# Kernel optimization log

Hardware: AMD Instinct MI355X
Metric: run time of the kernel (lower is better)

The kernel has to match this reference:

```python
import jax, jax.numpy as jnp
import numpy as np

N = 2800        # real node count (before hardcoded pad)
NPAD = 3000     # module pads node dim to 3000
F_IN = 8192     # node_features
H1 = 256        # dim_h1 (GCLSTM in_channels)
H2 = 128        # GCLSTM out_channels
E = 179200      # edges (avg degree 64)


def setup_inputs() -> dict:
    key = jax.random.key(0)
    ks = jax.random.split(key, 12)
    inp = {
        "x": jax.random.normal(ks[0], (N, F_IN), jnp.float32),
        "edge_index": jax.random.randint(ks[1], (2, E), 0, N, dtype=jnp.int64),
        "edge_weight": jax.random.uniform(ks[2], (E,), jnp.float32),
        "h0": jax.random.normal(ks[3], (NPAD, H2), jnp.float32),
        "c0": jax.random.normal(ks[4], (NPAD, H2), jnp.float32),
        # fc0: node_features -> dim_h1
        "fc0_w": jax.random.normal(ks[5], (F_IN, H1), jnp.float32) / np.float32(np.sqrt(F_IN)),
        "fc0_b": jnp.zeros((H1,), jnp.float32),
        # GCLSTM gate params, stacked over gates [i, f, c, o]
        "Wx": jax.random.normal(ks[6], (4, H1, H2), jnp.float32) / np.float32(np.sqrt(H1)),
        "bg": jnp.zeros((4, H2), jnp.float32),
        # ChebConv (K=2) weights per gate: theta_0, theta_1, bias
        "cw0": jax.random.normal(ks[7], (4, H2, H2), jnp.float32) / np.float32(np.sqrt(H2)),
        "cw1": jax.random.normal(ks[8], (4, H2, H2), jnp.float32) / np.float32(np.sqrt(H2)),
        "cb": jnp.zeros((4, H2), jnp.float32),
        # final fc: 128 -> 1
        "fc_w": jax.random.normal(ks[9], (H2, 1), jnp.float32) / np.float32(np.sqrt(H2)),
        "fc_b": jnp.zeros((1,), jnp.float32),
    }
    return inp


def _cheb_scaled_laplacian(edge_index, edge_weight, num_nodes):
    # ChebConv 'sym' norm with lambda_max=2: L_hat = -D^{-1/2} A D^{-1/2}
    # (diagonal of scaled Laplacian cancels to zero with fill_value=-1 self loops)
    row, col = edge_index[0], edge_index[1]
    deg = jax.ops.segment_sum(edge_weight, row, num_segments=num_nodes)
    dinv = jnp.where(deg > 0, jax.lax.rsqrt(jnp.where(deg > 0, deg, 1.0)), 0.0)
    return -dinv[row] * edge_weight * dinv[col]  # per-edge weight of L_hat


def reference(x, edge_weight, h0, c0, fc0_w, fc0_b, Wx, bg, cw0, cw1, cb,
              fc_w, fc_b, edge_index):
    n_real = x.shape[0]
    # hardcoded zero-padding of node dim to 3000
    xp = jnp.concatenate([x, jnp.zeros((NPAD - n_real, x.shape[1]), x.dtype)], axis=0)
    z = jax.nn.relu(xp @ fc0_w + fc0_b)                       # [3000, 256]

    row, col = edge_index[0], edge_index[1]
    w_hat = _cheb_scaled_laplacian(edge_index, edge_weight, NPAD)
    # Chebyshev T1 term: L_hat @ H  (shared across all four gates)
    T1 = jax.ops.segment_sum(w_hat[:, None] * h0[row], col, num_segments=NPAD)  # [3000,128]

    # all four gate pre-activations at once: X W_x + ChebConv(H) + b
    gates = (jnp.einsum('nf,gfo->gno', z, Wx)
             + jnp.einsum('nd,gdo->gno', h0, cw0)
             + jnp.einsum('nd,gdo->gno', T1, cw1)
             + (bg + cb)[:, None, :])                          # [4, 3000, 128]

    i = jax.nn.sigmoid(gates[0])
    f = jax.nn.sigmoid(gates[1])
    t = jnp.tanh(gates[2])
    o = jax.nn.sigmoid(gates[3])
    c_new = f * c0 + i * t
    h_new = o * jnp.tanh(c_new)                                # [3000, 128]

    out = (jax.nn.relu(h_new) @ fc_w + fc_b)[:, 0]             # squeeze last dim
    out = out[:n_real]                                         # drop padding rows
    return out, h_new
```

## Files before the change

kernel.cpp:

```cpp
#include <hip/hip_runtime.h>
#include <math.h>

#define N_REAL 2800
#define NPAD   3000
#define F_IN   8192
#define H1     256
#define H2     128
#define NE     179200
#define UDIM   512
#define NGATE  512
#define MPAD   3072
#define SPLITK 16
#define KCH    (F_IN / SPLITK)
#define NHB    64
#define EPB    (NE / NHB)

typedef _Float16 half8_t __attribute__((ext_vector_type(8)));
typedef _Float16 half4_t __attribute__((ext_vector_type(4)));
typedef float    floatx4 __attribute__((ext_vector_type(4)));

__device__ __forceinline__ void async_g2l_16(const _Float16* g, _Float16* l) {
    __builtin_amdgcn_global_load_lds(
        (const __attribute__((address_space(1))) unsigned int*)g,
        (__attribute__((address_space(3))) unsigned int*)l, 16, 0, 0);
}

__global__ __launch_bounds__(256)
void prep_kernel(const float* __restrict__ w, const float* __restrict__ Wx,
                 const float* __restrict__ cw0, const float* __restrict__ cw1,
                 const float* __restrict__ bg, const float* __restrict__ cb,
                 const float* __restrict__ h0, const int* __restrict__ ei,
                 const float* __restrict__ ew,
                 _Float16* __restrict__ wTp, _Float16* __restrict__ Wcp,
                 float* __restrict__ biasv, _Float16* __restrict__ U16,
                 float* __restrict__ deg, int* __restrict__ counts,
                 int* __restrict__ cnt_pT) {
    __shared__ __align__(16) char pmem[24576];
    int b = blockIdx.x;
    int t = threadIdx.x;
    if (b < NHB) {
        float* sdeg = (float*)pmem;
        int*   scnt = (int*)(pmem + 12288);
        for (int i = t; i < 3072; i += 256) { sdeg[i] = 0.f; scnt[i] = 0; }
        __syncthreads();
        int e0 = b * EPB;
        for (int i = t; i < EPB; i += 256) {
            int e = e0 + i;
            atomicAdd(&sdeg[ei[e]], ew[e]);
            atomicAdd(&scnt[ei[NE + e]], 1);
        }
        __syncthreads();
        for (int i = t; i < 3072; i += 256) {
            atomicAdd(&deg[i], sdeg[i]);
            atomicAdd(&counts[i], scnt[i]);
            cnt_pT[i * NHB + b] = scnt[i];
        }
    } else if (b < 2112) {
        float (*tile)[33] = (float(*)[33])pmem;
        int bb = b - NHB;
        int k0 = (bb & 255) * 32;
        int n0 = (bb >> 8) * 32;
        int tx = t & 31, ty = t >> 5;
#pragma unroll
        for (int r = 0; r < 4; r++)
            tile[ty + r * 8][tx] = w[(size_t)(k0 + ty + r * 8) * H1 + n0 + tx];
        __syncthreads();
        if (t < 128) {
            int u_l = t >> 5;
            int n_l = t & 31;
            half8_t h;
#pragma unroll
            for (int j = 0; j < 8; j++) h[j] = (_Float16)tile[u_l * 8 + j][n_l];
            *(half8_t*)&wTp[(((size_t)(k0 >> 3) + u_l) * H1 + n0 + n_l) * 8] = h;
        }
    } else if (b < 3136) {
        int idx = (b - 2112) * 256 + t;
        if (idx < UDIM * NGATE) {
            int col = idx >> 9;
            int f   = idx & 511;
            int g = col >> 7, o = col & 127;
            float v;
            if (f < H1)            v = Wx[((size_t)g * H1 + f) * H2 + o];
            else if (f < H1 + H2)  v = cw0[((size_t)g * H2 + (f - H1)) * H2 + o];
            else                   v = cw1[((size_t)g * H2 + (f - H1 - H2)) * H2 + o];
            Wcp[(((size_t)(f >> 3)) * NGATE + col) * 8 + (f & 7)] = (_Float16)v;
            if (f == 0) biasv[col] = bg[col] + cb[col];
        }
    } else {
        int q = (b - 3136) * 256 + t;
        int m = q >> 5;
        int o4 = (q & 31) * 4;
        half4_t h = {};
        if (m < NPAD) {
            float4 v = *(const float4*)&h0[(size_t)m * H2 + o4];
            h[0] = (_Float16)v.x; h[1] = (_Float16)v.y; h[2] = (_Float16)v.z; h[3] = (_Float16)v.w;
        }
        *(half4_t*)&U16[(size_t)m * UDIM + H1 + o4] = h;
    }
}

__global__ __launch_bounds__(256, 3)
void gemm1_fused(const float* __restrict__ x, const _Float16* __restrict__ wTp,
                 float* __restrict__ P) {
    __shared__ __align__(16) _Float16 As[8][64][8];
    __shared__ __align__(16) _Float16 Bs[8][256][8];
    const int t = threadIdx.x;
    const int wave = t >> 6, lane = t & 63;
    const int l16 = lane & 15, u4 = lane >> 4;
    const int m0 = blockIdx.x * 64;
    const int kbase = blockIdx.y * KCH;

    const int arow = t >> 2;
    const int aseg = t & 3;
    const bool avalid = (m0 + arow) < N_REAL;
    const float* agp = x + (size_t)(m0 + arow) * F_IN + kbase + aseg * 16;

    floatx4 acc[4][4] = {};

    float4 a0 = make_float4(0.f, 0.f, 0.f, 0.f), a1 = a0, a2 = a0, a3 = a0;
    if (avalid) {
        a0 = *(const float4*)(agp + 0);
        a1 = *(const float4*)(agp + 4);
        a2 = *(const float4*)(agp + 8);
        a3 = *(const float4*)(agp + 12);
    }

    for (int kk = 0; kk < KCH; kk += 64) {
        const _Float16* bbase = wTp + ((size_t)((kbase + kk) >> 3)) * (H1 * 8);
#pragma unroll
        for (int q = 0; q < 2; q++) {
            int u = wave * 2 + q;
#pragma unroll
            for (int rg = 0; rg < 4; rg++)
                async_g2l_16(bbase + ((size_t)u * H1 + rg * 64 + lane) * 8,
                             &Bs[u][rg * 64 + lane][0]);
        }
        half8_t hlo, hhi;
        hlo[0] = (_Float16)a0.x; hlo[1] = (_Float16)a0.y; hlo[2] = (_Float16)a0.z; hlo[3] = (_Float16)a0.w;
        hlo[4] = (_Float16)a1.x; hlo[5] = (_Float16)a1.y; hlo[6] = (_Float16)a1.z; hlo[7] = (_Float16)a1.w;
        hhi[0] = (_Float16)a2.x; hhi[1] = (_Float16)a2.y; hhi[2] = (_Float16)a2.z; hhi[3] = (_Float16)a2.w;
        hhi[4] = (_Float16)a3.x; hhi[5] = (_Float16)a3.y; hhi[6] = (_Float16)a3.z; hhi[7] = (_Float16)a3.w;
        *(half8_t*)&As[aseg * 2][arow][0]     = hlo;
        *(half8_t*)&As[aseg * 2 + 1][arow][0] = hhi;
        __syncthreads();
        if (kk + 64 < KCH && avalid) {
            a0 = *(const float4*)(agp + kk + 64);
            a1 = *(const float4*)(agp + kk + 68);
            a2 = *(const float4*)(agp + kk + 72);
            a3 = *(const float4*)(agp + kk + 76);
        }
#pragma unroll
        for (int ks = 0; ks < 2; ks++) {
            half8_t a[4], bfr[4];
#pragma unroll
            for (int i = 0; i < 4; i++) a[i] = *(const half8_t*)&As[ks * 4 + u4][i * 16 + l16][0];
#pragma unroll
            for (int j = 0; j < 4; j++) bfr[j] = *(const half8_t*)&Bs[ks * 4 + u4][wave * 64 + j * 16 + l16][0];
#pragma unroll
            for (int i = 0; i < 4; i++)
#pragma unroll
                for (int j = 0; j < 4; j++)
                    acc[i][j] = __builtin_amdgcn_mfma_f32_16x16x32_f16(a[i], bfr[j], acc[i][j], 0, 0, 0);
        }
        __syncthreads();
    }

    float* Pb = P + ((size_t)blockIdx.y * MPAD + m0) * H1;
#pragma unroll
    for (int i = 0; i < 4; i++)
#pragma unroll
        for (int j = 0; j < 4; j++) {
            int n = wave * 64 + j * 16 + l16;
#pragma unroll
            for (int r = 0; r < 4; r++)
                Pb[(size_t)(i * 16 + u4 * 4 + r) * H1 + n] = acc[i][j][r];
        }
}

__device__ __forceinline__ void zreduce_body(int zb, int t, const float* __restrict__ P,
                                             const float* __restrict__ fc0_b,
                                             _Float16* __restrict__ U16) {
    int q = zb * 256 + t;
    int m = q >> 6;
    int n4 = (q & 63) * 4;
    float s0 = 0.f, s1 = 0.f, s2 = 0.f, s3 = 0.f;
#pragma unroll
    for (int sk = 0; sk < SPLITK; sk++) {
        float4 p = *(const float4*)&P[((size_t)sk * MPAD + m) * H1 + n4];
        s0 += p.x; s1 += p.y; s2 += p.z; s3 += p.w;
    }
    float4 bb = *(const float4*)&fc0_b[n4];
    half4_t h;
    h[0] = (_Float16)fmaxf(s0 + bb.x, 0.f);
    h[1] = (_Float16)fmaxf(s1 + bb.y, 0.f);
    h[2] = (_Float16)fmaxf(s2 + bb.z, 0.f);
    h[3] = (_Float16)fmaxf(s3 + bb.w, 0.f);
    *(half4_t*)&U16[(size_t)m * UDIM + n4] = h;
}

__global__ __launch_bounds__(256)
void scanz_kernel(const int* __restrict__ counts, const float* __restrict__ deg,
                  int* __restrict__ offsets, float* __restrict__ dinv,
                  const int* __restrict__ cnt_pT, int* __restrict__ base_rel,
                  const float* __restrict__ P, const float* __restrict__ fc0_b,
                  _Float16* __restrict__ U16) {
    int b = blockIdx.x;
    int t = threadIdx.x;
    if (b == 0) {
        __shared__ int wt[4];
        int i0 = t * 12;
        int v[12];
        int s = 0;
#pragma unroll
        for (int j = 0; j < 12; j++) { v[j] = counts[i0 + j]; s += v[j]; }
        int incl = s;
#pragma unroll
        for (int d = 1; d < 64; d <<= 1) {
            int n = __shfl_up(incl, d);
            if ((t & 63) >= d) incl += n;
        }
        if ((t & 63) == 63) wt[t >> 6] = incl;
        __syncthreads();
        int wbase = 0;
#pragma unroll
        for (int w = 0; w < 4; w++) wbase += (w < (t >> 6)) ? wt[w] : 0;
        int run = wbase + incl - s;
#pragma unroll
        for (int j = 0; j < 12; j++) { offsets[i0 + j] = run; run += v[j]; }
        for (int i = t; i < NPAD; i += 256) {
            float d = deg[i];
            dinv[i] = (d > 0.f) ? rsqrtf(d) : 0.f;
        }
    } else if (b <= 12) {
        int j = (b - 1) * 256 + t;
        const int* src = cnt_pT + (size_t)j * NHB;
        int* dst = base_rel + (size_t)j * NHB;
        int run = 0;
#pragma unroll
        for (int bb = 0; bb < NHB; bb++) { dst[bb] = run; run += src[bb]; }
    } else {
        zreduce_body(b - 13, t, P, fc0_b, U16);
    }
}

__global__ __launch_bounds__(256)
void scatz_kernel(const int* __restrict__ ei, const int* __restrict__ offsets,
                  const int* __restrict__ base_rel, int* __restrict__ eid,
                  const float* __restrict__ P, const float* __restrict__ fc0_b,
                  _Float16* __restrict__ U16) {
    int b = blockIdx.x;
    int t = threadIdx.x;
    if (b < NHB) {
        __shared__ int sb[3072];
        for (int j = t; j < 3072; j += 256)
            sb[j] = offsets[j] + base_rel[(size_t)j * NHB + b];
        __syncthreads();
        int e0 = b * EPB;
        for (int i = t; i < EPB; i += 256) {
            int e = e0 + i;
            int c = ei[NE + e];
            int p = atomicAdd(&sb[c], 1);
            eid[p] = e;
        }
    } else {
        zreduce_body(384 + (b - NHB), t, P, fc0_b, U16);
    }
}

__global__ __launch_bounds__(128)
void gather_kernel(const int* __restrict__ ei, const float* __restrict__ ew,
                   const float* __restrict__ h0, const float* __restrict__ dinv,
                   const int* __restrict__ offsets, const int* __restrict__ eid,
                   _Float16* __restrict__ U16) {
    __shared__ int   sr[128];
    __shared__ float sw[128];
    int n = blockIdx.x;
    int t = threadIdx.x;
    int beg = offsets[n], end = offsets[n + 1];
    float dc = dinv[n];
    float acc = 0.f;
    for (int base = beg; base < end; base += 128) {
        int j = base + t;
        if (j < end) {
            int e = eid[j];
            int r = ei[e];
            sr[t] = r;
            sw[t] = -dinv[r] * ew[e];
        }
        __syncthreads();
        int cnt = min(128, end - base);
        int k = 0;
        for (; k + 8 <= cnt; k += 8) {
            int   r0 = sr[k],   r1 = sr[k+1], r2 = sr[k+2], r3 = sr[k+3];
            int   r4 = sr[k+4], r5 = sr[k+5], r6 = sr[k+6], r7 = sr[k+7];
            float w0 = sw[k],   w1 = sw[k+1], w2 = sw[k+2], w3 = sw[k+3];
            float w4 = sw[k+4], w5 = sw[k+5], w6 = sw[k+6], w7 = sw[k+7];
            float v0 = h0[(size_t)r0 * H2 + t];
            float v1 = h0[(size_t)r1 * H2 + t];
            float v2 = h0[(size_t)r2 * H2 + t];
            float v3 = h0[(size_t)r3 * H2 + t];
            float v4 = h0[(size_t)r4 * H2 + t];
            float v5 = h0[(size_t)r5 * H2 + t];
            float v6 = h0[(size_t)r6 * H2 + t];
            float v7 = h0[(size_t)r7 * H2 + t];
            acc += w0 * v0 + w1 * v1 + w2 * v2 + w3 * v3
                 + w4 * v4 + w5 * v5 + w6 * v6 + w7 * v7;
        }
        for (; k < cnt; k++)
            acc += sw[k] * h0[(size_t)sr[k] * H2 + t];
        __syncthreads();
    }
    U16[(size_t)n * UDIM + H1 + H2 + t] = (_Float16)(acc * dc);
}

__global__ __launch_bounds__(256, 3)
void gemm2_mfma(const _Float16* __restrict__ U16, const _Float16* __restrict__ Wcp,
                float* __restrict__ gatesP) {
    __shared__ __align__(16) _Float16 As[8][64][8];
    __shared__ __align__(16) _Float16 Bs[8][256][8];
    const int t = threadIdx.x;
    const int wave = t >> 6, lane = t & 63;
    const int l16 = lane & 15, u4 = lane >> 4;
    const int n0 = blockIdx.x * 256;
    const int m0 = blockIdx.y * 64;
    const int kz = blockIdx.z * 256;

    floatx4 acc[4][4] = {};

    for (int kk = kz; kk < kz + 256; kk += 64) {
        const _Float16* bbase = Wcp + ((size_t)(kk >> 3)) * (NGATE * 8);
#pragma unroll
        for (int q = 0; q < 2; q++) {
            int u = wave * 2 + q;
            async_g2l_16(U16 + (size_t)(m0 + lane) * UDIM + kk + u * 8, &As[u][lane][0]);
#pragma unroll
            for (int rg = 0; rg < 4; rg++)
                async_g2l_16(bbase + ((size_t)u * NGATE + n0 + rg * 64 + lane) * 8,
                             &Bs[u][rg * 64 + lane][0]);
        }
        __syncthreads();
#pragma unroll
        for (int ks = 0; ks < 2; ks++) {
            half8_t a[4], bfr[4];
#pragma unroll
            for (int i = 0; i < 4; i++) a[i] = *(const half8_t*)&As[ks * 4 + u4][i * 16 + l16][0];
#pragma unroll
            for (int j = 0; j < 4; j++) bfr[j] = *(const half8_t*)&Bs[ks * 4 + u4][wave * 64 + j * 16 + l16][0];
#pragma unroll
            for (int i = 0; i < 4; i++)
#pragma unroll
                for (int j = 0; j < 4; j++)
                    acc[i][j] = __builtin_amdgcn_mfma_f32_16x16x32_f16(a[i], bfr[j], acc[i][j], 0, 0, 0);
        }
        __syncthreads();
    }

    float* g = gatesP + (size_t)blockIdx.z * MPAD * NGATE;
#pragma unroll
    for (int i = 0; i < 4; i++)
#pragma unroll
        for (int j = 0; j < 4; j++) {
            int n = n0 + wave * 64 + j * 16 + l16;
#pragma unroll
            for (int r = 0; r < 4; r++)
                g[(size_t)(m0 + i * 16 + u4 * 4 + r) * NGATE + n] = acc[i][j][r];
        }
}

__global__ __launch_bounds__(128)
void lstm_kernel(const float* __restrict__ gates, const float* __restrict__ c0,
                 const float* __restrict__ biasv, const float* __restrict__ fc_w,
                 const float* __restrict__ fc_b, float* __restrict__ out) {
    __shared__ float red[2];
    int n = blockIdx.x;
    int o = threadIdx.x;
    const float* g0 = gates + (size_t)n * NGATE;
    const float* g1 = g0 + (size_t)MPAD * NGATE;
    float gi = g0[o]          + g1[o]          + biasv[o];
    float gf = g0[H2 + o]     + g1[H2 + o]     + biasv[H2 + o];
    float gt = g0[2 * H2 + o] + g1[2 * H2 + o] + biasv[2 * H2 + o];
    float go = g0[3 * H2 + o] + g1[3 * H2 + o] + biasv[3 * H2 + o];
    float iv = 1.f / (1.f + expf(-gi));
    float fv = 1.f / (1.f + expf(-gf));
    float tv = tanhf(gt);
    float ov = 1.f / (1.f + expf(-go));
    float c = fv * c0[(size_t)n * H2 + o] + iv * tv;
    float h = ov * tanhf(c);
    out[N_REAL + (size_t)n * H2 + o] = h;

    float r = fmaxf(h, 0.f) * fc_w[o];
#pragma unroll
    for (int s = 32; s; s >>= 1) r += __shfl_down(r, s);
    if ((o & 63) == 0) red[o >> 6] = r;
    __syncthreads();
    if (o == 0 && n < N_REAL) out[n] = red[0] + red[1] + fc_b[0];
}

extern "C" void kernel_launch(void* const* d_in, const int* in_sizes, int n_in,
                              void* d_out, int out_size, void* d_ws, size_t ws_size,
                              hipStream_t stream) {
    const float* x     = (const float*)d_in[0];
    const int*   ei    = (const int*)d_in[1];
    const float* ew    = (const float*)d_in[2];
    const float* h0    = (const float*)d_in[3];
    const float* c0    = (const float*)d_in[4];
    const float* fc0_w = (const float*)d_in[5];
    const float* fc0_b = (const float*)d_in[6];
    const float* Wx    = (const float*)d_in[7];
    const float* bg    = (const float*)d_in[8];
    const float* cw0   = (const float*)d_in[9];
    const float* cw1   = (const float*)d_in[10];
    const float* cb    = (const float*)d_in[11];
    const float* fc_w  = (const float*)d_in[12];
    const float* fc_b  = (const float*)d_in[13];
    float* out = (float*)d_out;

    float* P        = (float*)d_ws;
    float* gates    = P + (size_t)SPLITK * MPAD * H1;
    float* biasv    = gates + 2 * (size_t)MPAD * NGATE;
    float* dinv     = biasv + NGATE;
    float* deg      = dinv + 3072;
    int*   counts   = (int*)(deg + 3072);
    int*   offs     = counts + 3072;
    int*   cnt_pT   = offs + 3072;
    int*   base_rel = cnt_pT + 3072 * NHB;
    int*   eid      = base_rel + 3072 * NHB;
    _Float16* U16 = (_Float16*)(((uintptr_t)(eid + NE) + 255) & ~(uintptr_t)255);
    _Float16* Wcp = U16 + (size_t)MPAD * UDIM;
    _Float16* wTp = Wcp + (size_t)UDIM * NGATE;

    hipMemsetAsync(deg, 0, 2 * 3072 * sizeof(float), stream);
    prep_kernel<<<3520, 256, 0, stream>>>(fc0_w, Wx, cw0, cw1, bg, cb, h0, ei, ew,
                                          wTp, Wcp, biasv, U16, deg, counts, cnt_pT);
    gemm1_fused<<<dim3(MPAD / 64, SPLITK), 256, 0, stream>>>(x, wTp, P);
    scanz_kernel<<<397, 256, 0, stream>>>(counts, deg, offs, dinv, cnt_pT, base_rel, P, fc0_b, U16);
    scatz_kernel<<<NHB + 384, 256, 0, stream>>>(ei, offs, base_rel, eid, P, fc0_b, U16);
    gather_kernel<<<NPAD, 128, 0, stream>>>(ei, ew, h0, dinv, offs, eid, U16);
    gemm2_mfma<<<dim3(NGATE / 256, MPAD / 64, 2), 256, 0, stream>>>(U16, Wcp, gates);
    lstm_kernel<<<NPAD, 128, 0, stream>>>(gates, c0, biasv, fc_w, fc_b, out);
}
```

Before: 242.9 us.

## Double-buffer gemm1, halve split-K, merge scan/scatter, fuse gemm2 with LSTM

The fc0 GEMM now uses double-buffered LDS with deeper A prefetch, and split-K drops from 16 to 8, which halves partial-sum traffic but also halves the number of blocks. The scan and scatter kernels are merged into one launch: each scatter block recomputes its own base from the per-block counts, so the base_rel buffer and one kernel launch go away. The gate GEMM now covers all 512 columns and the full K per block, and the LSTM pointwise math and final fc run in its epilogue from LDS. This removes the gates round-trip through global memory and the separate LSTM launch, at the cost of only 48 blocks at one block per CU for gemm2.

Measured after the change: 305.2 us. 1.26x slower.

```diff
diff --git a/kernel.cpp b/kernel.cpp
--- a/kernel.cpp
+++ b/kernel.cpp
@@ -10,7 +10,7 @@
 #define UDIM   512
 #define NGATE  512
 #define MPAD   3072
-#define SPLITK 16
+#define SPLITK 8
 #define KCH    (F_IN / SPLITK)
 #define NHB    64
 #define EPB    (NE / NHB)
@@ -99,11 +99,56 @@
     }
 }
 
-__global__ __launch_bounds__(256, 3)
+__device__ __forceinline__ void stage_b1(const _Float16* __restrict__ wTp,
+                                         _Float16 (*bs)[256][8], int wave, int lane, size_t kb8) {
+    const _Float16* bbase = wTp + kb8 * (H1 * 8);
+#pragma unroll
+    for (int q = 0; q < 2; q++) {
+        int u = wave * 2 + q;
+#pragma unroll
+        for (int rg = 0; rg < 4; rg++)
+            async_g2l_16(bbase + ((size_t)u * H1 + rg * 64 + lane) * 8,
+                         &bs[u][rg * 64 + lane][0]);
+    }
+}
+
+__device__ __forceinline__ void put_a1(_Float16 (*as)[64][8], int arow, int aseg,
+                                       const float4* A) {
+    half8_t hlo, hhi;
+    hlo[0] = (_Float16)A[0].x; hlo[1] = (_Float16)A[0].y; hlo[2] = (_Float16)A[0].z; hlo[3] = (_Float16)A[0].w;
+    hlo[4] = (_Float16)A[1].x; hlo[5] = (_Float16)A[1].y; hlo[6] = (_Float16)A[1].z; hlo[7] = (_Float16)A[1].w;
+    hhi[0] = (_Float16)A[2].x; hhi[1] = (_Float16)A[2].y; hhi[2] = (_Float16)A[2].z; hhi[3] = (_Float16)A[2].w;
+    hhi[4] = (_Float16)A[3].x; hhi[5] = (_Float16)A[3].y; hhi[6] = (_Float16)A[3].z; hhi[7] = (_Float16)A[3].w;
+    *(half8_t*)&as[aseg * 2][arow][0]     = hlo;
+    *(half8_t*)&as[aseg * 2 + 1][arow][0] = hhi;
+}
+
+__device__ __forceinline__ void comp64(floatx4 (&acc)[4][4], _Float16 (*as)[64][8],
+                                       _Float16 (*bs)[256][8], int wave, int u4, int l16) {
+#pragma unroll
+    for (int ks = 0; ks < 2; ks++) {
+        half8_t a[4], bfr[4];
+#pragma unroll
+        for (int i = 0; i < 4; i++) a[i] = *(const half8_t*)&as[ks * 4 + u4][i * 16 + l16][0];
+#pragma unroll
+        for (int j = 0; j < 4; j++) bfr[j] = *(const half8_t*)&bs[ks * 4 + u4][wave * 64 + j * 16 + l16][0];
+#pragma unroll
+        for (int i = 0; i < 4; i++)
+#pragma unroll
+            for (int j = 0; j < 4; j++)
+                acc[i][j] = __builtin_amdgcn_mfma_f32_16x16x32_f16(a[i], bfr[j], acc[i][j], 0, 0, 0);
+    }
+}
+
+#define LOADA1(A, off) do { if (avalid) { \
+    A[0] = *(const float4*)(agp + (off));      A[1] = *(const float4*)(agp + (off) + 4); \
+    A[2] = *(const float4*)(agp + (off) + 8);  A[3] = *(const float4*)(agp + (off) + 12); } } while (0)
+
+__global__ __launch_bounds__(256, 2)
 void gemm1_fused(const float* __restrict__ x, const _Float16* __restrict__ wTp,
                  float* __restrict__ P) {
-    __shared__ __align__(16) _Float16 As[8][64][8];
-    __shared__ __align__(16) _Float16 Bs[8][256][8];
+    __shared__ __align__(16) _Float16 As[2][8][64][8];
+    __shared__ __align__(16) _Float16 Bs[2][8][256][8];
     const int t = threadIdx.x;
     const int wave = t >> 6, lane = t & 63;
     const int l16 = lane & 15, u4 = lane >> 4;
@@ -116,52 +161,28 @@
     const float* agp = x + (size_t)(m0 + arow) * F_IN + kbase + aseg * 16;
 
     floatx4 acc[4][4] = {};
-
-    float4 a0 = make_float4(0.f, 0.f, 0.f, 0.f), a1 = a0, a2 = a0, a3 = a0;
-    if (avalid) {
-        a0 = *(const float4*)(agp + 0);
-        a1 = *(const float4*)(agp + 4);
-        a2 = *(const float4*)(agp + 8);
-        a3 = *(const float4*)(agp + 12);
-    }
-
-    for (int kk = 0; kk < KCH; kk += 64) {
-        const _Float16* bbase = wTp + ((size_t)((kbase + kk) >> 3)) * (H1 * 8);
-#pragma unroll
-        for (int q = 0; q < 2; q++) {
-            int u = wave * 2 + q;
-#pragma unroll
-            for (int rg = 0; rg < 4; rg++)
-                async_g2l_16(bbase + ((size_t)u * H1 + rg * 64 + lane) * 8,
-                             &Bs[u][rg * 64 + lane][0]);
-        }
-        half8_t hlo, hhi;
-        hlo[0] = (_Float16)a0.x; hlo[1] = (_Float16)a0.y; hlo[2] = (_Float16)a0.z; hlo[3] = (_Float16)a0.w;
-        hlo[4] = (_Float16)a1.x; hlo[5] = (_Float16)a1.y; hlo[6] = (_Float16)a1.z; hlo[7] = (_Float16)a1.w;
-        hhi[0] = (_Float16)a2.x; hhi[1] = (_Float16)a2.y; hhi[2] = (_Float16)a2.z; hhi[3] = (_Float16)a2.w;
-        hhi[4] = (_Float16)a3.x; hhi[5] = (_Float16)a3.y; hhi[6] = (_Float16)a3.z; hhi[7] = (_Float16)a3.w;
-        *(half8_t*)&As[aseg * 2][arow][0]     = hlo;
-        *(half8_t*)&As[aseg * 2 + 1][arow][0] = hhi;
-        __syncthreads();
-        if (kk + 64 < KCH && avalid) {
-            a0 = *(const float4*)(agp + kk + 64);
-            a1 = *(const float4*)(agp + kk + 68);
-            a2 = *(const float4*)(agp + kk + 72);
-            a3 = *(const float4*)(agp + kk + 76);
-        }
-#pragma unroll
-        for (int ks = 0; ks < 2; ks++) {
-            half8_t a[4], bfr[4];
-#pragma unroll
-            for (int i = 0; i < 4; i++) a[i] = *(const half8_t*)&As[ks * 4 + u4][i * 16 + l16][0];
-#pragma unroll
-            for (int j = 0; j < 4; j++) bfr[j] = *(const half8_t*)&Bs[ks * 4 + u4][wave * 64 + j * 16 + l16][0];
-#pragma unroll
-            for (int i = 0; i < 4; i++)
-#pragma unroll
-                for (int j = 0; j < 4; j++)
-                    acc[i][j] = __builtin_amdgcn_mfma_f32_16x16x32_f16(a[i], bfr[j], acc[i][j], 0, 0, 0);
-        }
+    float4 A0[4] = {}, A1[4] = {};
+
+    LOADA1(A0, 0);
+    stage_b1(wTp, Bs[0], wave, lane, (size_t)kbase >> 3);
+    put_a1(As[0], arow, aseg, A0);
+    LOADA1(A1, 64);
+    LOADA1(A0, 128);
+    __syncthreads();
+
+    for (int q8 = 0; q8 < 8; ++q8) {
+        const int k = 2 * q8;
+        stage_b1(wTp, Bs[1], wave, lane, (size_t)(kbase + (k + 1) * 64) >> 3);
+        put_a1(As[1], arow, aseg, A1);
+        if (q8 < 7) LOADA1(A1, (k + 3) * 64);
+        comp64(acc, As[0], Bs[0], wave, u4, l16);
+        __syncthreads();
+        if (q8 < 7) {
+            stage_b1(wTp, Bs[0], wave, lane, (size_t)(kbase + (k + 2) * 64) >> 3);
+            put_a1(As[0], arow, aseg, A0);
+            if (q8 < 6) LOADA1(A0, (k + 4) * 64);
+        }
+        comp64(acc, As[1], Bs[1], wave, u4, l16);
         __syncthreads();
     }
 
@@ -199,18 +220,19 @@
 }
 
 __global__ __launch_bounds__(256)
-void scanz_kernel(const int* __restrict__ counts, const float* __restrict__ deg,
-                  int* __restrict__ offsets, float* __restrict__ dinv,
-                  const int* __restrict__ cnt_pT, int* __restrict__ base_rel,
-                  const float* __restrict__ P, const float* __restrict__ fc0_b,
-                  _Float16* __restrict__ U16) {
+void scatterz_kernel(const int* __restrict__ ei, const int* __restrict__ counts,
+                     const float* __restrict__ deg, const int* __restrict__ cnt_pT,
+                     int* __restrict__ offsets, float* __restrict__ dinv,
+                     int* __restrict__ eid,
+                     const float* __restrict__ P, const float* __restrict__ fc0_b,
+                     _Float16* __restrict__ U16) {
+    __shared__ int sb[3072];
+    __shared__ int wt[4];
     int b = blockIdx.x;
     int t = threadIdx.x;
-    if (b == 0) {
-        __shared__ int wt[4];
+    if (b < NHB + 1) {
         int i0 = t * 12;
-        int v[12];
-        int s = 0;
+        int v[12]; int s = 0;
 #pragma unroll
         for (int j = 0; j < 12; j++) { v[j] = counts[i0 + j]; s += v[j]; }
         int incl = s;
@@ -225,45 +247,33 @@
 #pragma unroll
         for (int w = 0; w < 4; w++) wbase += (w < (t >> 6)) ? wt[w] : 0;
         int run = wbase + incl - s;
-#pragma unroll
-        for (int j = 0; j < 12; j++) { offsets[i0 + j] = run; run += v[j]; }
-        for (int i = t; i < NPAD; i += 256) {
-            float d = deg[i];
-            dinv[i] = (d > 0.f) ? rsqrtf(d) : 0.f;
-        }
-    } else if (b <= 12) {
-        int j = (b - 1) * 256 + t;
-        const int* src = cnt_pT + (size_t)j * NHB;
-        int* dst = base_rel + (size_t)j * NHB;
-        int run = 0;
-#pragma unroll
-        for (int bb = 0; bb < NHB; bb++) { dst[bb] = run; run += src[bb]; }
+        if (b < NHB) {
+#pragma unroll
+            for (int j = 0; j < 12; j++) {
+                int base = 0;
+                const int* cp = cnt_pT + (size_t)(i0 + j) * NHB;
+                for (int bb = 0; bb < b; bb++) base += cp[bb];
+                sb[i0 + j] = run + base;
+                run += v[j];
+            }
+            __syncthreads();
+            int e0 = b * EPB;
+            for (int i = t; i < EPB; i += 256) {
+                int e = e0 + i;
+                int c = ei[NE + e];
+                int p = atomicAdd(&sb[c], 1);
+                eid[p] = e;
+            }
+        } else {
+#pragma unroll
+            for (int j = 0; j < 12; j++) { offsets[i0 + j] = run; run += v[j]; }
+            for (int i = t; i < NPAD; i += 256) {
+                float d = deg[i];
+                dinv[i] = (d > 0.f) ? rsqrtf(d) : 0.f;
+            }
+        }
     } else {
-        zreduce_body(b - 13, t, P, fc0_b, U16);
-    }
-}
-
-__global__ __launch_bounds__(256)
-void scatz_kernel(const int* __restrict__ ei, const int* __restrict__ offsets,
-                  const int* __restrict__ base_rel, int* __restrict__ eid,
-                  const float* __restrict__ P, const float* __restrict__ fc0_b,
-                  _Float16* __restrict__ U16) {
-    int b = blockIdx.x;
-    int t = threadIdx.x;
-    if (b < NHB) {
-        __shared__ int sb[3072];
-        for (int j = t; j < 3072; j += 256)
-            sb[j] = offsets[j] + base_rel[(size_t)j * NHB + b];
-        __syncthreads();
-        int e0 = b * EPB;
-        for (int i = t; i < EPB; i += 256) {
-            int e = e0 + i;
-            int c = ei[NE + e];
-            int p = atomicAdd(&sb[c], 1);
-            eid[p] = e;
-        }
-    } else {
-        zreduce_body(384 + (b - NHB), t, P, fc0_b, U16);
+        zreduce_body(b - NHB - 1, t, P, fc0_b, U16);
     }
 }
 
@@ -313,87 +323,90 @@
     U16[(size_t)n * UDIM + H1 + H2 + t] = (_Float16)(acc * dc);
 }
 
-__global__ __launch_bounds__(256, 3)
-void gemm2_mfma(const _Float16* __restrict__ U16, const _Float16* __restrict__ Wcp,
-                float* __restrict__ gatesP) {
-    __shared__ __align__(16) _Float16 As[8][64][8];
-    __shared__ __align__(16) _Float16 Bs[8][256][8];
+__global__ __launch_bounds__(256, 1)
+void gemm2lstm(const _Float16* __restrict__ U16, const _Float16* __restrict__ Wcp,
+               const float* __restrict__ c0, const float* __restrict__ biasv,
+               const float* __restrict__ fc_w, const float* __restrict__ fc_b,
+               float* __restrict__ out) {
+    __shared__ __align__(16) char smem[73728];
+    _Float16 (*As)[64][8]  = (_Float16(*)[64][8])smem;
+    _Float16 (*Bs)[512][8] = (_Float16(*)[512][8])(smem + 8192);
     const int t = threadIdx.x;
     const int wave = t >> 6, lane = t & 63;
     const int l16 = lane & 15, u4 = lane >> 4;
-    const int n0 = blockIdx.x * 256;
-    const int m0 = blockIdx.y * 64;
-    const int kz = blockIdx.z * 256;
-
-    floatx4 acc[4][4] = {};
-
-    for (int kk = kz; kk < kz + 256; kk += 64) {
+    const int m0 = blockIdx.x * 64;
+
+    floatx4 acc[4][8] = {};
+
+    for (int kk = 0; kk < UDIM; kk += 64) {
         const _Float16* bbase = Wcp + ((size_t)(kk >> 3)) * (NGATE * 8);
 #pragma unroll
         for (int q = 0; q < 2; q++) {
             int u = wave * 2 + q;
             async_g2l_16(U16 + (size_t)(m0 + lane) * UDIM + kk + u * 8, &As[u][lane][0]);
 #pragma unroll
-            for (int rg = 0; rg < 4; rg++)
-                async_g2l_16(bbase + ((size_t)u * NGATE + n0 + rg * 64 + lane) * 8,
+            for (int rg = 0; rg < 8; rg++)
+                async_g2l_16(bbase + ((size_t)u * NGATE + rg * 64 + lane) * 8,
                              &Bs[u][rg * 64 + lane][0]);
         }
         __syncthreads();
 #pragma unroll
         for (int ks = 0; ks < 2; ks++) {
-            half8_t a[4], bfr[4];
+            half8_t a[4], bfr[8];
 #pragma unroll
             for (int i = 0; i < 4; i++) a[i] = *(const half8_t*)&As[ks * 4 + u4][i * 16 + l16][0];
 #pragma unroll
-            for (int j = 0; j < 4; j++) bfr[j] = *(const half8_t*)&Bs[ks * 4 + u4][wave * 64 + j * 16 + l16][0];
+            for (int j = 0; j < 8; j++) bfr[j] = *(const half8_t*)&Bs[ks * 4 + u4][wave * 128 + j * 16 + l16][0];
 #pragma unroll
             for (int i = 0; i < 4; i++)
 #pragma unroll
-                for (int j = 0; j < 4; j++)
+                for (int j = 0; j < 8; j++)
                     acc[i][j] = __builtin_amdgcn_mfma_f32_16x16x32_f16(a[i], bfr[j], acc[i][j], 0, 0, 0);
         }
         __syncthreads();
     }
 
-    float* g = gatesP + (size_t)blockIdx.z * MPAD * NGATE;
-#pragma unroll
-    for (int i = 0; i < 4; i++)
-#pragma unroll
-        for (int j = 0; j < 4; j++) {
-            int n = n0 + wave * 64 + j * 16 + l16;
-#pragma unroll
-            for (int r = 0; r < 4; r++)
-                g[(size_t)(m0 + i * 16 + u4 * 4 + r) * NGATE + n] = acc[i][j][r];
-        }
-}
-
-__global__ __launch_bounds__(128)
-void lstm_kernel(const float* __restrict__ gates, const float* __restrict__ c0,
-                 const float* __restrict__ biasv, const float* __restrict__ fc_w,
-                 const float* __restrict__ fc_b, float* __restrict__ out) {
-    __shared__ float red[2];
-    int n = blockIdx.x;
-    int o = threadIdx.x;
-    const float* g0 = gates + (size_t)n * NGATE;
-    const float* g1 = g0 + (size_t)MPAD * NGATE;
-    float gi = g0[o]          + g1[o]          + biasv[o];
-    float gf = g0[H2 + o]     + g1[H2 + o]     + biasv[H2 + o];
-    float gt = g0[2 * H2 + o] + g1[2 * H2 + o] + biasv[2 * H2 + o];
-    float go = g0[3 * H2 + o] + g1[3 * H2 + o] + biasv[3 * H2 + o];
-    float iv = 1.f / (1.f + expf(-gi));
-    float fv = 1.f / (1.f + expf(-gf));
-    float tv = tanhf(gt);
-    float ov = 1.f / (1.f + expf(-go));
-    float c = fv * c0[(size_t)n * H2 + o] + iv * tv;
-    float h = ov * tanhf(c);
-    out[N_REAL + (size_t)n * H2 + o] = h;
-
-    float r = fmaxf(h, 0.f) * fc_w[o];
-#pragma unroll
-    for (int s = 32; s; s >>= 1) r += __shfl_down(r, s);
-    if ((o & 63) == 0) red[o >> 6] = r;
-    __syncthreads();
-    if (o == 0 && n < N_REAL) out[n] = red[0] + red[1] + fc_b[0];
+    float* sg = (float*)smem;
+#pragma unroll
+    for (int h = 0; h < 2; ++h) {
+#pragma unroll
+        for (int ii = 0; ii < 2; ii++) {
+            int i = h * 2 + ii;
+#pragma unroll
+            for (int j = 0; j < 8; j++)
+#pragma unroll
+                for (int r = 0; r < 4; r++)
+                    sg[(ii * 16 + u4 * 4 + r) * 516 + wave * 128 + j * 16 + l16] = acc[i][j][r];
+        }
+        __syncthreads();
+        int r = t >> 3;
+        int og = t & 7;
+        int n = m0 + h * 32 + r;
+        float rsum = 0.f;
+        if (n < NPAD) {
+#pragma unroll
+            for (int k2 = 0; k2 < 16; k2++) {
+                int o = og + k2 * 8;
+                float gi = sg[r * 516 + o]       + biasv[o];
+                float gf = sg[r * 516 + 128 + o] + biasv[128 + o];
+                float gt = sg[r * 516 + 256 + o] + biasv[256 + o];
+                float go = sg[r * 516 + 384 + o] + biasv[384 + o];
+                float iv = 1.f / (1.f + expf(-gi));
+                float fv = 1.f / (1.f + expf(-gf));
+                float tv = tanhf(gt);
+                float ov = 1.f / (1.f + expf(-go));
+                float c = fv * c0[(size_t)n * H2 + o] + iv * tv;
+                float hh = ov * tanhf(c);
+                out[N_REAL + (size_t)n * H2 + o] = hh;
+                rsum += fmaxf(hh, 0.f) * fc_w[o];
+            }
+        }
+        rsum += __shfl_down(rsum, 4);
+        rsum += __shfl_down(rsum, 2);
+        rsum += __shfl_down(rsum, 1);
+        if ((t & 7) == 0 && n < N_REAL) out[n] = rsum + fc_b[0];
+        __syncthreads();
+    }
 }
 
 extern "C" void kernel_launch(void* const* d_in, const int* in_sizes, int n_in,
@@ -416,15 +429,13 @@
     float* out = (float*)d_out;
 
     float* P        = (float*)d_ws;
-    float* gates    = P + (size_t)SPLITK * MPAD * H1;
-    float* biasv    = gates + 2 * (size_t)MPAD * NGATE;
+    float* biasv    = P + (size_t)SPLITK * MPAD * H1;
     float* dinv     = biasv + NGATE;
     float* deg      = dinv + 3072;
     int*   counts   = (int*)(deg + 3072);
     int*   offs     = counts + 3072;
     int*   cnt_pT   = offs + 3072;
-    int*   base_rel = cnt_pT + 3072 * NHB;
-    int*   eid      = base_rel + 3072 * NHB;
+    int*   eid      = cnt_pT + 3072 * NHB;
     _Float16* U16 = (_Float16*)(((uintptr_t)(eid + NE) + 255) & ~(uintptr_t)255);
     _Float16* Wcp = U16 + (size_t)MPAD * UDIM;
     _Float16* wTp = Wcp + (size_t)UDIM * NGATE;
@@ -433,9 +444,8 @@
     prep_kernel<<<3520, 256, 0, stream>>>(fc0_w, Wx, cw0, cw1, bg, cb, h0, ei, ew,
                                           wTp, Wcp, biasv, U16, deg, counts, cnt_pT);
     gemm1_fused<<<dim3(MPAD / 64, SPLITK), 256, 0, stream>>>(x, wTp, P);
-    scanz_kernel<<<397, 256, 0, stream>>>(counts, deg, offs, dinv, cnt_pT, base_rel, P, fc0_b, U16);
-    scatz_kernel<<<NHB + 384, 256, 0, stream>>>(ei, offs, base_rel, eid, P, fc0_b, U16);
+    scatterz_kernel<<<NHB + 1 + 768, 256, 0, stream>>>(ei, counts, deg, cnt_pT, offs, dinv,
+                                                       eid, P, fc0_b, U16);
     gather_kernel<<<NPAD, 128, 0, stream>>>(ei, ew, h0, dinv, offs, eid, U16);
-    gemm2_mfma<<<dim3(NGATE / 256, MPAD / 64, 2), 256, 0, stream>>>(U16, Wcp, gates);
-    lstm_kernel<<<NPAD, 128, 0, stream>>>(gates, c0, biasv, fc_w, fc_b, out);
-}
+    gemm2lstm<<<MPAD / 64, 256, 0, stream>>>(U16, Wcp, c0, biasv, fc_w, fc_b, out);
+}
```
